# Kernel tuning notes

Hardware: AMD Instinct MI355X
Metric: run time of the kernel (lower is better)

Reference implementation:

```python
import jax, jax.numpy as jnp
import numpy as np

N = 50000       # nodes
E = 800000      # edges (before self-loops)
F_IN = 128      # in_channels
HID = 32        # hidden_channels per head
HEADS = 4
OUT = 16        # out_channels
NEG_SLOPE = 0.2 # PyG GATConv leaky_relu slope
EPS = 1e-16     # PyG softmax denominator eps
BN_EPS = 1e-5


def setup_inputs() -> dict:
    key = jax.random.key(0)
    ks = jax.random.split(key, 20)
    rn = lambda k, shp, s=0.1: (jax.random.normal(k, shp, jnp.float32) * s)
    x = jax.random.normal(ks[0], (N, F_IN), jnp.float32)
    edge_index = jax.random.randint(ks[1], (2, E), 0, N, dtype=jnp.int32)
    D0 = HEADS * HID  # 128
    return {
        "x": x, "edge_index": edge_index,
        # layer 0: GATConv(F_IN -> HID, heads=HEADS, concat=True)
        "W0": rn(ks[2], (F_IN, HEADS * HID)), "as0": rn(ks[3], (HEADS, HID)),
        "ad0": rn(ks[4], (HEADS, HID)), "b0": jnp.zeros((D0,), jnp.float32),
        "g0": jnp.ones((D0,), jnp.float32) + rn(ks[5], (D0,), 0.05),
        "be0": rn(ks[6], (D0,), 0.05),
        # layer 1: GATConv(D0 -> HID, heads=HEADS, concat=True)
        "W1": rn(ks[7], (D0, HEADS * HID)), "as1": rn(ks[8], (HEADS, HID)),
        "ad1": rn(ks[9], (HEADS, HID)), "b1": jnp.zeros((D0,), jnp.float32),
        "g1": jnp.ones((D0,), jnp.float32) + rn(ks[10], (D0,), 0.05),
        "be1": rn(ks[11], (D0,), 0.05),
        # layer 2: GATConv(D0 -> OUT, heads=1, concat=False)
        "W2": rn(ks[12], (D0, OUT)), "as2": rn(ks[13], (1, OUT)),
        "ad2": rn(ks[14], (1, OUT)), "b2": jnp.zeros((OUT,), jnp.float32),
    }


def _gat(x, src, dst, W, a_s, a_d, b, heads, ch, concat):
    n = x.shape[0]
    h = (x @ W).reshape(n, heads, ch)                       # [N,H,C]
    score_s = (h * a_s).sum(-1)                             # [N,H]
    score_d = (h * a_d).sum(-1)                             # [N,H]
    e = jax.nn.leaky_relu(score_s[src] + score_d[dst], NEG_SLOPE)  # [E,H]
    emax = jax.ops.segment_max(e, dst, num_segments=n)
    emax = jnp.where(jnp.isfinite(emax), emax, 0.0)
    p = jnp.exp(e - emax[dst])
    denom = jax.ops.segment_sum(p, dst, num_segments=n)
    alpha = p / (denom[dst] + EPS)                          # segment softmax over dst
    out = jax.ops.segment_sum(h[src] * alpha[:, :, None], dst, num_segments=n)
    out = out.reshape(n, heads * ch) if concat else out.mean(axis=1)
    return out + b


def _bn(x, g, be):
    m = x.mean(0)
    v = x.var(0)
    return (x - m) * jax.lax.rsqrt(v + BN_EPS) * g + be


def reference(x, edge_index, W0, as0, ad0, b0, g0, be0,
              W1, as1, ad1, b1, g1, be1, W2, as2, ad2, b2):
    n = x.shape[0]
    loop = jnp.arange(n, dtype=edge_index.dtype)
    src = jnp.concatenate([edge_index[0], loop])  # PyG add_self_loops
    dst = jnp.concatenate([edge_index[1], loop])
    h = _gat(x, src, dst, W0, as0, ad0, b0, HEADS, HID, True)
    h = jax.nn.elu(_bn(h, g0, be0))                 # dropout disabled (eval)
    h = _gat(h, src, dst, W1, as1, ad1, b1, HEADS, HID, True)
    h = jax.nn.elu(_bn(h, g1, be1))
    return _gat(h, src, dst, W2, as2, ad2, b2, 1, OUT, False)
```

## Files before the change

### kernel.cpp

```cpp
#include <hip/hip_runtime.h>
#include <hip/hip_bf16.h>
#include <math.h>

#define NEG_SLOPE 0.2f
#define EPS_SM 1e-16f
#define BN_EPS 1e-5f
#define CHUNKS 256

typedef __attribute__((ext_vector_type(8))) short bf16x8;
typedef __attribute__((ext_vector_type(4))) float f32x4;

__device__ __forceinline__ float lrelu(float x) { return x > 0.f ? x : NEG_SLOPE * x; }
__device__ __forceinline__ ushort f2bf(float f) {
    uint u = __float_as_uint(f);
    return (ushort)((u + 0x7FFFu + ((u >> 16) & 1u)) >> 16);
}
__device__ __forceinline__ float bfl(uint u) { return __uint_as_float(u << 16); }
__device__ __forceinline__ float bfh(uint u) { return __uint_as_float(u & 0xFFFF0000u); }

__global__ void pack_w(const float* __restrict__ W0, const float* __restrict__ W1,
                       const float* __restrict__ W2, ushort* __restrict__ P0,
                       ushort* __restrict__ P1, ushort* __restrict__ P2) {
    int i = blockIdx.x * blockDim.x + threadIdx.x;
    const float* W;
    ushort* P;
    int NC, s;
    if (i < 16384) { W = W0; P = P0; NC = 128; s = i; }
    else if (i < 32768) { W = W1; P = P1; NC = 128; s = i - 16384; }
    else if (i < 34816) { W = W2; P = P2; NC = 16; s = i - 32768; }
    else return;
    int k = s / NC, col = s % NC;
    int CT = NC >> 4;
    int dst = (((k >> 5) * CT + (col >> 4)) << 9) +
              (((col & 15) | (((k >> 3) & 3) << 4)) << 3) + (k & 7);
    P[dst] = f2bf(W[s]);
}

__global__ __launch_bounds__(256) void bucket_count(const int* __restrict__ dst, int E,
                                                    int* __restrict__ hist, int nbuck) {
    __shared__ int h[256];
    int blk = blockIdx.x, tid = threadIdx.x;
    h[tid] = 0;
    __syncthreads();
    int e0 = (int)(((long)E * blk) >> 8);
    int e1 = (int)(((long)E * (blk + 1)) >> 8);
    for (int i = e0 + tid; i < e1; i += 256) atomicAdd(&h[dst[i] >> 8], 1);
    __syncthreads();
    if (tid < nbuck) hist[tid * CHUNKS + blk] = h[tid];
}

__global__ __launch_bounds__(256) void bucket_scatter(const int* __restrict__ src,
                                                      const int* __restrict__ dst, int E,
                                                      const int* __restrict__ base,
                                                      uint* __restrict__ bpack, int nbuck) {
    __shared__ int cur[256];
    int blk = blockIdx.x, tid = threadIdx.x;
    if (tid < nbuck) cur[tid] = base[tid * CHUNKS + blk];
    __syncthreads();
    int e0 = (int)(((long)E * blk) >> 8);
    int e1 = (int)(((long)E * (blk + 1)) >> 8);
    for (int i = e0 + tid; i < e1; i += 256) {
        int d = dst[i];
        int p = atomicAdd(&cur[d >> 8], 1);
        bpack[p] = ((uint)src[i] << 8) | (uint)(d & 255);
    }
}

__global__ __launch_bounds__(256) void fine_csr(const uint* __restrict__ bpack,
                                                const int* __restrict__ base, int E, int n,
                                                int* __restrict__ offs, int* __restrict__ srcs,
                                                int nbuck) {
    __shared__ int cnt[256];
    __shared__ int wsum[4];
    int bk = blockIdx.x, tid = threadIdx.x;
    int ebase = base[bk * CHUNKS];
    int eend = base[(bk + 1) * CHUNKS];
    cnt[tid] = 0;
    __syncthreads();
    for (int i = ebase + tid; i < eend; i += 256) atomicAdd(&cnt[bpack[i] & 255], 1);
    __syncthreads();
    int lane = tid & 63, w = tid >> 6;
    int v = cnt[tid];
    int incl = v;
#pragma unroll
    for (int d = 1; d < 64; d <<= 1) {
        int t = __shfl_up(incl, d, 64);
        if (lane >= d) incl += t;
    }
    if (lane == 63) wsum[w] = incl;
    __syncthreads();
    int wbase = 0;
    for (int j = 0; j < w; ++j) wbase += wsum[j];
    int excl = wbase + incl - v;
    int node = bk * 256 + tid;
    if (node < n) offs[node] = ebase + excl;
    cnt[tid] = ebase + excl;
    __syncthreads();
    for (int i = ebase + tid; i < eend; i += 256) {
        uint pk = bpack[i];
        int p = atomicAdd(&cnt[pk & 255], 1);
        srcs[p] = (int)(pk >> 8);
    }
    if (bk == nbuck - 1 && tid == 0) offs[n] = E;
}

template <int NC, int HEADS, bool XBN>
__global__ __launch_bounds__(64) void gemm_mfma(
    const void* __restrict__ Xv, const ushort* __restrict__ Wp, ushort* __restrict__ Hb,
    int n, const float* __restrict__ sumsP, const float* __restrict__ g,
    const float* __restrict__ be, const float* __restrict__ as_, const float* __restrict__ ad_,
    float* __restrict__ ss, float* __restrict__ sd) {
    int tid = threadIdx.x;
    constexpr int CT = NC / 16;
    constexpr int FPH = NC / HEADS / 16;
    __shared__ __align__(16) ushort Xb[16 * 128];
    __shared__ float ssl[16 * HEADS], sdl[16 * HEADS];
    int row0 = (int)blockIdx.x * 16;
    if constexpr (!XBN) {
        const float* X = (const float*)Xv;
#pragma unroll
        for (int i = 0; i < 8; ++i) {
            int idx = tid + i * 64;
            int row = idx >> 5, q = idx & 31;
            int gr = row0 + row;
            float4 v = make_float4(0.f, 0.f, 0.f, 0.f);
            if (gr < n) v = ((const float4*)(X + (long)gr * 128))[q];
            ushort4 p = make_ushort4(f2bf(v.x), f2bf(v.y), f2bf(v.z), f2bf(v.w));
            int s = (q >> 1) ^ (row & 15);
            *(ushort4*)&Xb[row * 128 + s * 8 + (q & 1) * 4] = p;
        }
    } else {
        const ushort* X = (const ushort*)Xv;
        int c8 = (tid & 15) * 8;
        float inv_n = 1.f / (float)n;
        float bm[8], bs[8], bb[8];
#pragma unroll
        for (int j = 0; j < 8; ++j) {
            int ch = c8 + j;
            float m = sumsP[ch * 16] * inv_n;
            float vv = fmaxf(sumsP[(128 + ch) * 16] * inv_n - m * m, 0.f);
            bm[j] = m;
            bs[j] = rsqrtf(vv + BN_EPS) * g[ch];
            bb[j] = be[ch];
        }
#pragma unroll
        for (int i = 0; i < 4; ++i) {
            int idx = tid + i * 64;
            int row = idx >> 4, g8 = idx & 15;
            int gr = row0 + row;
            uint4 v = make_uint4(0, 0, 0, 0);
            if (gr < n) v = ((const uint4*)(X + (long)gr * 128))[g8];
            float a, b;
#define BNE(comp, j0)                                                  \
    a = bfl(comp); b = bfh(comp);                                      \
    a = (a - bm[j0]) * bs[j0] + bb[j0]; a = a > 0.f ? a : expm1f(a);   \
    b = (b - bm[j0 + 1]) * bs[j0 + 1] + bb[j0 + 1];                    \
    b = b > 0.f ? b : expm1f(b);                                       \
    comp = (uint)f2bf(a) | ((uint)f2bf(b) << 16);
            BNE(v.x, 0) BNE(v.y, 2) BNE(v.z, 4) BNE(v.w, 6)
#undef BNE
            int s = g8 ^ (row & 15);
            *(uint4*)&Xb[row * 128 + s * 8] = v;
        }
    }
    __syncthreads();
    int lane = tid;
    int lrow = lane & 15, lhi = lane >> 4;
    f32x4 zero = {0.f, 0.f, 0.f, 0.f};
    f32x4 acc[CT];
#pragma unroll
    for (int f = 0; f < CT; ++f) acc[f] = zero;
    const ushort* xr = &Xb[lrow * 128];
#pragma unroll
    for (int ks = 0; ks < 4; ++ks) {
        int kg = ks * 4 + lhi;
        bf16x8 a = *(const bf16x8*)&xr[(kg ^ lrow) << 3];
#pragma unroll
        for (int f = 0; f < CT; ++f) {
            bf16x8 b = *(const bf16x8*)&Wp[((ks * CT + f) * 64 + lane) * 8];
            acc[f] = __builtin_amdgcn_mfma_f32_16x16x32_bf16(a, b, acc[f], 0, 0, 0);
        }
    }
    __syncthreads();
#pragma unroll
    for (int f = 0; f < CT; ++f)
#pragma unroll
        for (int j = 0; j < 4; ++j)
            Xb[(lhi * 4 + j) * NC + f * 16 + lrow] = f2bf(acc[f][j]);
    float asv[CT], adv[CT];
#pragma unroll
    for (int f = 0; f < CT; ++f) {
        asv[f] = as_[f * 16 + lrow];
        adv[f] = ad_[f * 16 + lrow];
    }
#pragma unroll
    for (int h = 0; h < HEADS; ++h) {
        float ps[4] = {}, pd[4] = {};
#pragma unroll
        for (int fi = 0; fi < FPH; ++fi) {
            int f = h * FPH + fi;
#pragma unroll
            for (int j = 0; j < 4; ++j) {
                ps[j] = fmaf(acc[f][j], asv[f], ps[j]);
                pd[j] = fmaf(acc[f][j], adv[f], pd[j]);
            }
        }
#pragma unroll
        for (int j = 0; j < 4; ++j) {
#pragma unroll
            for (int d = 1; d < 16; d <<= 1) {
                ps[j] += __shfl_xor(ps[j], d, 64);
                pd[j] += __shfl_xor(pd[j], d, 64);
            }
            if (lrow == 0) {
                ssl[(lhi * 4 + j) * HEADS + h] = ps[j];
                sdl[(lhi * 4 + j) * HEADS + h] = pd[j];
            }
        }
    }
    __syncthreads();
    constexpr int NU = 16 * NC / 8;
#pragma unroll
    for (int i = 0; i < (NU + 63) / 64; ++i) {
        int idx = tid + i * 64;
        if (idx < NU) {
            int row = idx / (NC / 8), c8i = idx % (NC / 8);
            int gr = row0 + row;
            if (gr < n) ((uint4*)&Hb[(long)gr * NC])[c8i] = ((const uint4*)Xb)[idx];
        }
    }
    if (tid < 16 * HEADS) {
        int row = tid / HEADS, hh = tid % HEADS;
        int gr = row0 + row;
        if (gr < n) {
            ss[(long)gr * HEADS + hh] = ssl[tid];
            sd[(long)gr * HEADS + hh] = sdl[tid];
        }
    }
}

__global__ __launch_bounds__(1024) void scan_kernel(const int* __restrict__ deg,
                                                    int* __restrict__ offs, int n) {
    __shared__ int wsum[16];
    __shared__ int wpre[16];
    __shared__ int carry_s;
    int tid = threadIdx.x;
    int lane = tid & 63;
    int w = tid >> 6;
    if (tid == 0) carry_s = 0;
    __syncthreads();
    int nv = (n + 3) >> 2;
    for (int base = 0; base < nv; base += 1024) {
        int carry = carry_s;
        int gi = base + tid;
        int e0 = gi * 4;
        int4 v = make_int4(0, 0, 0, 0);
        if (e0 + 3 < n) {
            v = ((const int4*)deg)[gi];
        } else if (e0 < n) {
            v.x = deg[e0];
            if (e0 + 1 < n) v.y = deg[e0 + 1];
            if (e0 + 2 < n) v.z = deg[e0 + 2];
        }
        int tsum = v.x + v.y + v.z + v.w;
        int incl = tsum;
#pragma unroll
        for (int d = 1; d < 64; d <<= 1) {
            int t = __shfl_up(incl, d, 64);
            if (lane >= d) incl += t;
        }
        if (lane == 63) wsum[w] = incl;
        __syncthreads();
        if (w == 0 && lane < 16) {
            int s = wsum[lane];
#pragma unroll
            for (int d = 1; d < 16; d <<= 1) {
                int t = __shfl_up(s, d, 64);
                if (lane >= d) s += t;
            }
            wpre[lane] = s;
        }
        __syncthreads();
        int wbase = (w == 0) ? 0 : wpre[w - 1];
        int ex = carry + wbase + incl - tsum;
        if (e0 < n) {
            int4 o;
            o.x = ex;
            o.y = ex + v.x;
            o.z = o.y + v.y;
            o.w = o.z + v.z;
            if (e0 + 3 < n) {
                ((int4*)offs)[gi] = o;
            } else {
                offs[e0] = o.x;
                if (e0 + 1 < n) offs[e0 + 1] = o.y;
                if (e0 + 2 < n) offs[e0 + 2] = o.z;
            }
        }
        __syncthreads();
        if (tid == 1023) carry_s = carry + wpre[15];
        __syncthreads();
    }
    if (tid == 0) offs[n] = carry_s;
}

__global__ __launch_bounds__(256) void gat_gather4(
    const uint* __restrict__ hb, const float* __restrict__ ss, const float* __restrict__ sd,
    const int* __restrict__ offs, const int* __restrict__ srcs,
    const float* __restrict__ bias, ushort* __restrict__ outb, int n) {
    int wid = threadIdx.x >> 6;
    int lane = threadIdx.x & 63;
    int node = blockIdx.x * 4 + wid;
    if (node >= n) return;
    int off = offs[node];
    int dg = offs[node + 1] - off;
    int grp = lane >> 4;
    int ll = lane & 15;
    int hd = ll >> 2;
    float sdn = sd[node * 4 + hd];
    float es = lrelu(ss[node * 4 + hd] + sdn);
    const uint* hrow = hb + ll * 4;
    float acc[8] = {};
    float sm = 0.f;
    int i = grp;
    for (; i + 4 < dg; i += 8) {
        int s0 = srcs[off + i];
        int s1 = srcs[off + i + 4];
        float w0 = __expf(lrelu(ss[s0 * 4 + hd] + sdn));
        float w1 = __expf(lrelu(ss[s1 * 4 + hd] + sdn));
        uint4 h0 = *(const uint4*)(hrow + (long)s0 * 64);
        uint4 h1 = *(const uint4*)(hrow + (long)s1 * 64);
        sm += w0 + w1;
        acc[0] = fmaf(w0, bfl(h0.x), acc[0]); acc[0] = fmaf(w1, bfl(h1.x), acc[0]);
        acc[1] = fmaf(w0, bfh(h0.x), acc[1]); acc[1] = fmaf(w1, bfh(h1.x), acc[1]);
        acc[2] = fmaf(w0, bfl(h0.y), acc[2]); acc[2] = fmaf(w1, bfl(h1.y), acc[2]);
        acc[3] = fmaf(w0, bfh(h0.y), acc[3]); acc[3] = fmaf(w1, bfh(h1.y), acc[3]);
        acc[4] = fmaf(w0, bfl(h0.z), acc[4]); acc[4] = fmaf(w1, bfl(h1.z), acc[4]);
        acc[5] = fmaf(w0, bfh(h0.z), acc[5]); acc[5] = fmaf(w1, bfh(h1.z), acc[5]);
        acc[6] = fmaf(w0, bfl(h0.w), acc[6]); acc[6] = fmaf(w1, bfl(h1.w), acc[6]);
        acc[7] = fmaf(w0, bfh(h0.w), acc[7]); acc[7] = fmaf(w1, bfh(h1.w), acc[7]);
    }
    for (; i < dg; i += 4) {
        int s = srcs[off + i];
        float w = __expf(lrelu(ss[s * 4 + hd] + sdn));
        sm += w;
        uint4 hv = *(const uint4*)(hrow + (long)s * 64);
        acc[0] = fmaf(w, bfl(hv.x), acc[0]);
        acc[1] = fmaf(w, bfh(hv.x), acc[1]);
        acc[2] = fmaf(w, bfl(hv.y), acc[2]);
        acc[3] = fmaf(w, bfh(hv.y), acc[3]);
        acc[4] = fmaf(w, bfl(hv.z), acc[4]);
        acc[5] = fmaf(w, bfh(hv.z), acc[5]);
        acc[6] = fmaf(w, bfl(hv.w), acc[6]);
        acc[7] = fmaf(w, bfh(hv.w), acc[7]);
    }
#pragma unroll
    for (int j = 0; j < 8; ++j) {
        acc[j] += __shfl_xor(acc[j], 16, 64);
        acc[j] += __shfl_xor(acc[j], 32, 64);
    }
    sm += __shfl_xor(sm, 16, 64);
    sm += __shfl_xor(sm, 32, 64);
    float wS = __expf(es);
    sm += wS;
    uint4 hvS = *(const uint4*)(hrow + (long)node * 64);
    acc[0] = fmaf(wS, bfl(hvS.x), acc[0]);
    acc[1] = fmaf(wS, bfh(hvS.x), acc[1]);
    acc[2] = fmaf(wS, bfl(hvS.y), acc[2]);
    acc[3] = fmaf(wS, bfh(hvS.y), acc[3]);
    acc[4] = fmaf(wS, bfl(hvS.z), acc[4]);
    acc[5] = fmaf(wS, bfh(hvS.z), acc[5]);
    acc[6] = fmaf(wS, bfl(hvS.w), acc[6]);
    acc[7] = fmaf(wS, bfh(hvS.w), acc[7]);
    float inv = 1.f / (sm + EPS_SM);
    if (grp == 0) {
        float4 bA = *(const float4*)&bias[ll * 8];
        float4 bB = *(const float4*)&bias[ll * 8 + 4];
        uint4 p;
        p.x = (uint)f2bf(acc[0] * inv + bA.x) | ((uint)f2bf(acc[1] * inv + bA.y) << 16);
        p.y = (uint)f2bf(acc[2] * inv + bA.z) | ((uint)f2bf(acc[3] * inv + bA.w) << 16);
        p.z = (uint)f2bf(acc[4] * inv + bB.x) | ((uint)f2bf(acc[5] * inv + bB.y) << 16);
        p.w = (uint)f2bf(acc[6] * inv + bB.z) | ((uint)f2bf(acc[7] * inv + bB.w) << 16);
        *(uint4*)&outb[(long)node * 128 + ll * 8] = p;
    }
}

__global__ __launch_bounds__(256) void gat_gather1(
    const uint* __restrict__ hb2, const float* __restrict__ ss, const float* __restrict__ sd,
    const int* __restrict__ offs, const int* __restrict__ srcs,
    const float* __restrict__ bias, float* __restrict__ out, int n) {
    int wid = threadIdx.x >> 6;
    int lane = threadIdx.x & 63;
    int node = blockIdx.x * 4 + wid;
    if (node >= n) return;
    int off = offs[node];
    int dg = offs[node + 1] - off;
    int grp = lane >> 3;
    int ll = lane & 7;
    float sdn = sd[node];
    float es = lrelu(ss[node] + sdn);
    float a0 = 0.f, a1 = 0.f, sm = 0.f;
    int i = grp;
    for (; i + 8 < dg; i += 16) {
        int s0 = srcs[off + i];
        int s1 = srcs[off + i + 8];
        float w0 = __expf(lrelu(ss[s0] + sdn));
        float w1 = __expf(lrelu(ss[s1] + sdn));
        uint h0 = hb2[s0 * 8 + ll];
        uint h1 = hb2[s1 * 8 + ll];
        sm += w0 + w1;
        a0 = fmaf(w0, bfl(h0), a0); a0 = fmaf(w1, bfl(h1), a0);
        a1 = fmaf(w0, bfh(h0), a1); a1 = fmaf(w1, bfh(h1), a1);
    }
    for (; i < dg; i += 8) {
        int s = srcs[off + i];
        float w = __expf(lrelu(ss[s] + sdn));
        sm += w;
        uint hv = hb2[s * 8 + ll];
        a0 = fmaf(w, bfl(hv), a0);
        a1 = fmaf(w, bfh(hv), a1);
    }
#pragma unroll
    for (int d = 8; d <= 32; d <<= 1) {
        a0 += __shfl_xor(a0, d, 64);
        a1 += __shfl_xor(a1, d, 64);
        sm += __shfl_xor(sm, d, 64);
    }
    float wS = __expf(es);
    sm += wS;
    uint hvS = hb2[node * 8 + ll];
    a0 = fmaf(wS, bfl(hvS), a0);
    a1 = fmaf(wS, bfh(hvS), a1);
    float inv = 1.f / (sm + EPS_SM);
    if (grp == 0) {
        float2 o = make_float2(a0 * inv + bias[ll * 2], a1 * inv + bias[ll * 2 + 1]);
        *(float2*)&out[(long)node * 16 + ll * 2] = o;
    }
}

__global__ __launch_bounds__(256) void bn_stats_bf16(const uint4* __restrict__ X4,
                                                     float* __restrict__ sumsP, int n) {
    __shared__ float red[4096];
    int tid = threadIdx.x;
    float s[8] = {}, s2[8] = {};
    long tot = (long)n * 16;
    long T = (long)gridDim.x * 256;
    for (long i = (long)blockIdx.x * 256 + tid; i < tot; i += T) {
        uint4 v = X4[i];
        float f;
        f = bfl(v.x); s[0] += f; s2[0] = fmaf(f, f, s2[0]);
        f = bfh(v.x); s[1] += f; s2[1] = fmaf(f, f, s2[1]);
        f = bfl(v.y); s[2] += f; s2[2] = fmaf(f, f, s2[2]);
        f = bfh(v.y); s[3] += f; s2[3] = fmaf(f, f, s2[3]);
        f = bfl(v.z); s[4] += f; s2[4] = fmaf(f, f, s2[4]);
        f = bfh(v.z); s[5] += f; s2[5] = fmaf(f, f, s2[5]);
        f = bfl(v.w); s[6] += f; s2[6] = fmaf(f, f, s2[6]);
        f = bfh(v.w); s[7] += f; s2[7] = fmaf(f, f, s2[7]);
    }
#pragma unroll
    for (int j = 0; j < 8; ++j) {
        red[j * 256 + tid] = s[j];
        red[(8 + j) * 256 + tid] = s2[j];
    }
    __syncthreads();
    int ch = tid & 127, st = tid >> 7;
    int base = (st * 8 + (ch & 7)) * 256 + (ch >> 3);
    float a = 0.f;
#pragma unroll
    for (int rep = 0; rep < 16; ++rep) a += red[base + rep * 16];
    atomicAdd(&sumsP[tid * 16], a);
}

extern "C" void kernel_launch(void* const* d_in, const int* in_sizes, int n_in,
                              void* d_out, int out_size, void* d_ws, size_t ws_size,
                              hipStream_t stream) {
    const float* x = (const float*)d_in[0];
    const int* ei = (const int*)d_in[1];
    const float* W0 = (const float*)d_in[2];
    const float* as0 = (const float*)d_in[3];
    const float* ad0 = (const float*)d_in[4];
    const float* b0 = (const float*)d_in[5];
    const float* g0 = (const float*)d_in[6];
    const float* be0 = (const float*)d_in[7];
    const float* W1 = (const float*)d_in[8];
    const float* as1 = (const float*)d_in[9];
    const float* ad1 = (const float*)d_in[10];
    const float* b1 = (const float*)d_in[11];
    const float* g1 = (const float*)d_in[12];
    const float* be1 = (const float*)d_in[13];
    const float* W2 = (const float*)d_in[14];
    const float* as2 = (const float*)d_in[15];
    const float* ad2 = (const float*)d_in[16];
    const float* b2 = (const float*)d_in[17];

    int n = in_sizes[0] / 128;
    int E = in_sizes[1] / 2;
    const int* srcA = ei;
    const int* dstA = ei + E;
    int nbuck = (n + 255) >> 8;

    char* base = (char*)d_ws;
    auto alloc = [&](size_t bytes) {
        char* p = base;
        base += (bytes + 255) & ~(size_t)255;
        return p;
    };
    ushort* hb = (ushort*)alloc((size_t)n * 128 * 2);
    ushort* actb = (ushort*)alloc((size_t)n * 128 * 2);
    ushort* h2b = (ushort*)alloc((size_t)n * 16 * 2);
    float* ssb = (float*)alloc((size_t)n * 4 * 4);
    float* sdb = (float*)alloc((size_t)n * 4 * 4);
    float* sumsP0 = (float*)alloc(4096 * 4);
    float* sumsP1 = (float*)alloc(4096 * 4);
    int* hist = (int*)alloc(((size_t)nbuck * CHUNKS + 1) * 4);
    int* bbase = (int*)alloc(((size_t)nbuck * CHUNKS + 1) * 4);
    uint* bpack = (uint*)alloc((size_t)E * 4);
    int* offs = (int*)alloc(((size_t)n + 1) * 4);
    int* srcs = (int*)alloc((size_t)E * 4);
    ushort* Wp0 = (ushort*)alloc(16384 * 2);
    ushort* Wp1 = (ushort*)alloc(16384 * 2);
    ushort* Wp2 = (ushort*)alloc(2048 * 2);

    float* out = (float*)d_out;

    hipMemsetAsync(sumsP0, 0, 4096 * 4 * 2, stream);

    pack_w<<<136, 256, 0, stream>>>(W0, W1, W2, Wp0, Wp1, Wp2);

    int gGemm = (n + 15) / 16;
    int gWave = (n + 3) / 4;

    gemm_mfma<128, 4, false><<<gGemm, 64, 0, stream>>>(
        x, Wp0, hb, n, nullptr, g0, be0, as0, ad0, ssb, sdb);

    bucket_count<<<CHUNKS, 256, 0, stream>>>(dstA, E, hist, nbuck);
    scan_kernel<<<1, 1024, 0, stream>>>(hist, bbase, nbuck * CHUNKS);
    bucket_scatter<<<CHUNKS, 256, 0, stream>>>(srcA, dstA, E, bbase, bpack, nbuck);
    fine_csr<<<nbuck, 256, 0, stream>>>(bpack, bbase, E, n, offs, srcs, nbuck);

    gat_gather4<<<gWave, 256, 0, stream>>>((const uint*)hb, ssb, sdb, offs, srcs, b0, actb, n);
    bn_stats_bf16<<<256, 256, 0, stream>>>((const uint4*)actb, sumsP0, n);

    gemm_mfma<128, 4, true><<<gGemm, 64, 0, stream>>>(
        actb, Wp1, hb, n, sumsP0, g0, be0, as1, ad1, ssb, sdb);
    gat_gather4<<<gWave, 256, 0, stream>>>((const uint*)hb, ssb, sdb, offs, srcs, b1, actb, n);
    bn_stats_bf16<<<256, 256, 0, stream>>>((const uint4*)actb, sumsP1, n);

    gemm_mfma<16, 1, true><<<gGemm, 64, 0, stream>>>(
        actb, Wp2, h2b, n, sumsP1, g1, be1, as2, ad2, ssb, sdb);
    gat_gather1<<<gWave, 256, 0, stream>>>((const uint*)h2b, ssb, sdb, offs, srcs, b2, out, n);
}
```

Measured before the change: 221.1 us.

## Store hidden features head-major and gather one head per block; fuse bucket count into GEMM

```diff
diff --git a/kernel.cpp b/kernel.cpp
--- a/kernel.cpp
+++ b/kernel.cpp
@@ -20,8 +20,10 @@
 
 __global__ void pack_w(const float* __restrict__ W0, const float* __restrict__ W1,
                        const float* __restrict__ W2, ushort* __restrict__ P0,
-                       ushort* __restrict__ P1, ushort* __restrict__ P2) {
+                       ushort* __restrict__ P1, ushort* __restrict__ P2,
+                       float* __restrict__ sums) {
     int i = blockIdx.x * blockDim.x + threadIdx.x;
+    if (i < 8192) sums[i] = 0.f;
     const float* W;
     ushort* P;
     int NC, s;
@@ -36,19 +38,6 @@
     P[dst] = f2bf(W[s]);
 }
 
-__global__ __launch_bounds__(256) void bucket_count(const int* __restrict__ dst, int E,
-                                                    int* __restrict__ hist, int nbuck) {
-    __shared__ int h[256];
-    int blk = blockIdx.x, tid = threadIdx.x;
-    h[tid] = 0;
-    __syncthreads();
-    int e0 = (int)(((long)E * blk) >> 8);
-    int e1 = (int)(((long)E * (blk + 1)) >> 8);
-    for (int i = e0 + tid; i < e1; i += 256) atomicAdd(&h[dst[i] >> 8], 1);
-    __syncthreads();
-    if (tid < nbuck) hist[tid * CHUNKS + blk] = h[tid];
-}
-
 __global__ __launch_bounds__(256) void bucket_scatter(const int* __restrict__ src,
                                                       const int* __restrict__ dst, int E,
                                                       const int* __restrict__ base,
@@ -104,18 +93,35 @@
     if (bk == nbuck - 1 && tid == 0) offs[n] = E;
 }
 
-template <int NC, int HEADS, bool XBN>
+template <int NC, int HEADS, bool XBN, bool BCFUSE>
 __global__ __launch_bounds__(64) void gemm_mfma(
     const void* __restrict__ Xv, const ushort* __restrict__ Wp, ushort* __restrict__ Hb,
     int n, const float* __restrict__ sumsP, const float* __restrict__ g,
     const float* __restrict__ be, const float* __restrict__ as_, const float* __restrict__ ad_,
-    float* __restrict__ ss, float* __restrict__ sd) {
+    float* __restrict__ ss, float* __restrict__ sd,
+    const int* __restrict__ dstE, int E, int* __restrict__ hist, int nbuck) {
     int tid = threadIdx.x;
     constexpr int CT = NC / 16;
     constexpr int FPH = NC / HEADS / 16;
+    constexpr int C = NC / HEADS;
     __shared__ __align__(16) ushort Xb[16 * 128];
     __shared__ float ssl[16 * HEADS], sdl[16 * HEADS];
-    int row0 = (int)blockIdx.x * 16;
+    if constexpr (BCFUSE) {
+        if ((int)blockIdx.x < CHUNKS) {
+            int* h = (int*)Xb;
+            for (int j = tid; j < 256; j += 64) h[j] = 0;
+            __syncthreads();
+            int blk = blockIdx.x;
+            int e0 = (int)(((long)E * blk) >> 8);
+            int e1 = (int)(((long)E * (blk + 1)) >> 8);
+            for (int i = e0 + tid; i < e1; i += 64) atomicAdd(&h[dstE[i] >> 8], 1);
+            __syncthreads();
+            for (int j = tid; j < nbuck; j += 64) hist[j * CHUNKS + blk] = h[j];
+            return;
+        }
+    }
+    int bid = BCFUSE ? ((int)blockIdx.x - CHUNKS) : (int)blockIdx.x;
+    int row0 = bid * 16;
     if constexpr (!XBN) {
         const float* X = (const float*)Xv;
 #pragma unroll
@@ -224,17 +230,19 @@
     for (int i = 0; i < (NU + 63) / 64; ++i) {
         int idx = tid + i * 64;
         if (idx < NU) {
-            int row = idx / (NC / 8), c8i = idx % (NC / 8);
+            int row = idx / (NC / 8), rem = idx % (NC / 8);
+            int head = rem / (C / 8), c8i = rem % (C / 8);
             int gr = row0 + row;
-            if (gr < n) ((uint4*)&Hb[(long)gr * NC])[c8i] = ((const uint4*)Xb)[idx];
+            if (gr < n)
+                ((uint4*)(Hb + ((long)head * n + gr) * C))[c8i] = ((const uint4*)Xb)[idx];
         }
     }
     if (tid < 16 * HEADS) {
         int row = tid / HEADS, hh = tid % HEADS;
         int gr = row0 + row;
         if (gr < n) {
-            ss[(long)gr * HEADS + hh] = ssl[tid];
-            sd[(long)gr * HEADS + hh] = sdl[tid];
+            ss[(long)hh * n + gr] = ssl[tid];
+            sd[(long)hh * n + gr] = sdl[tid];
         }
     }
 }
@@ -304,84 +312,74 @@
     if (tid == 0) offs[n] = carry_s;
 }
 
-__global__ __launch_bounds__(256) void gat_gather4(
-    const uint* __restrict__ hb, const float* __restrict__ ss, const float* __restrict__ sd,
+__global__ __launch_bounds__(256) void gat_gatherH(
+    const uint2* __restrict__ hbH, const float* __restrict__ ssT, const float* __restrict__ sdT,
     const int* __restrict__ offs, const int* __restrict__ srcs,
-    const float* __restrict__ bias, ushort* __restrict__ outb, int n) {
+    const float* __restrict__ bias, ushort* __restrict__ outb, int n, int nblk) {
     int wid = threadIdx.x >> 6;
     int lane = threadIdx.x & 63;
-    int node = blockIdx.x * 4 + wid;
+    int hd = blockIdx.x / nblk;
+    int nb = blockIdx.x - hd * nblk;
+    int node = nb * 4 + wid;
     if (node >= n) return;
+    long hn = (long)hd * n;
     int off = offs[node];
     int dg = offs[node + 1] - off;
-    int grp = lane >> 4;
-    int ll = lane & 15;
-    int hd = ll >> 2;
-    float sdn = sd[node * 4 + hd];
-    float es = lrelu(ss[node * 4 + hd] + sdn);
-    const uint* hrow = hb + ll * 4;
-    float acc[8] = {};
+    int grp = lane >> 3;
+    int ll = lane & 7;
+    float sdn = sdT[hn + node];
+    float es = lrelu(ssT[hn + node] + sdn);
+    const uint2* hrow = hbH + hn * 8 + ll;
+    const float* ssh = ssT + hn;
+    float acc[4] = {};
     float sm = 0.f;
     int i = grp;
-    for (; i + 4 < dg; i += 8) {
+    for (; i + 8 < dg; i += 16) {
         int s0 = srcs[off + i];
-        int s1 = srcs[off + i + 4];
-        float w0 = __expf(lrelu(ss[s0 * 4 + hd] + sdn));
-        float w1 = __expf(lrelu(ss[s1 * 4 + hd] + sdn));
-        uint4 h0 = *(const uint4*)(hrow + (long)s0 * 64);
-        uint4 h1 = *(const uint4*)(hrow + (long)s1 * 64);
+        int s1 = srcs[off + i + 8];
+        float w0 = __expf(lrelu(ssh[s0] + sdn));
+        float w1 = __expf(lrelu(ssh[s1] + sdn));
+        uint2 h0 = hrow[(long)s0 * 8];
+        uint2 h1 = hrow[(long)s1 * 8];
         sm += w0 + w1;
         acc[0] = fmaf(w0, bfl(h0.x), acc[0]); acc[0] = fmaf(w1, bfl(h1.x), acc[0]);
         acc[1] = fmaf(w0, bfh(h0.x), acc[1]); acc[1] = fmaf(w1, bfh(h1.x), acc[1]);
         acc[2] = fmaf(w0, bfl(h0.y), acc[2]); acc[2] = fmaf(w1, bfl(h1.y), acc[2]);
         acc[3] = fmaf(w0, bfh(h0.y), acc[3]); acc[3] = fmaf(w1, bfh(h1.y), acc[3]);
-        acc[4] = fmaf(w0, bfl(h0.z), acc[4]); acc[4] = fmaf(w1, bfl(h1.z), acc[4]);
-        acc[5] = fmaf(w0, bfh(h0.z), acc[5]); acc[5] = fmaf(w1, bfh(h1.z), acc[5]);
-        acc[6] = fmaf(w0, bfl(h0.w), acc[6]); acc[6] = fmaf(w1, bfl(h1.w), acc[6]);
-        acc[7] = fmaf(w0, bfh(h0.w), acc[7]); acc[7] = fmaf(w1, bfh(h1.w), acc[7]);
-    }
-    for (; i < dg; i += 4) {
+    }
+    for (; i < dg; i += 8) {
         int s = srcs[off + i];
-        float w = __expf(lrelu(ss[s * 4 + hd] + sdn));
+        float w = __expf(lrelu(ssh[s] + sdn));
         sm += w;
-        uint4 hv = *(const uint4*)(hrow + (long)s * 64);
+        uint2 hv = hrow[(long)s * 8];
         acc[0] = fmaf(w, bfl(hv.x), acc[0]);
         acc[1] = fmaf(w, bfh(hv.x), acc[1]);
         acc[2] = fmaf(w, bfl(hv.y), acc[2]);
         acc[3] = fmaf(w, bfh(hv.y), acc[3]);
-        acc[4] = fmaf(w, bfl(hv.z), acc[4]);
-        acc[5] = fmaf(w, bfh(hv.z), acc[5]);
-        acc[6] = fmaf(w, bfl(hv.w), acc[6]);
-        acc[7] = fmaf(w, bfh(hv.w), acc[7]);
-    }
-#pragma unroll
-    for (int j = 0; j < 8; ++j) {
+    }
+#pragma unroll
+    for (int j = 0; j < 4; ++j) {
+        acc[j] += __shfl_xor(acc[j], 8, 64);
         acc[j] += __shfl_xor(acc[j], 16, 64);
         acc[j] += __shfl_xor(acc[j], 32, 64);
     }
+    sm += __shfl_xor(sm, 8, 64);
     sm += __shfl_xor(sm, 16, 64);
     sm += __shfl_xor(sm, 32, 64);
     float wS = __expf(es);
     sm += wS;
-    uint4 hvS = *(const uint4*)(hrow + (long)node * 64);
+    uint2 hvS = hrow[(long)node * 8];
     acc[0] = fmaf(wS, bfl(hvS.x), acc[0]);
     acc[1] = fmaf(wS, bfh(hvS.x), acc[1]);
     acc[2] = fmaf(wS, bfl(hvS.y), acc[2]);
     acc[3] = fmaf(wS, bfh(hvS.y), acc[3]);
-    acc[4] = fmaf(wS, bfl(hvS.z), acc[4]);
-    acc[5] = fmaf(wS, bfh(hvS.z), acc[5]);
-    acc[6] = fmaf(wS, bfl(hvS.w), acc[6]);
-    acc[7] = fmaf(wS, bfh(hvS.w), acc[7]);
     float inv = 1.f / (sm + EPS_SM);
     if (grp == 0) {
-        float4 bA = *(const float4*)&bias[ll * 8];
-        float4 bB = *(const float4*)&bias[ll * 8 + 4];
-        uint4 p;
-        p.x = (uint)f2bf(acc[0] * inv + bA.x) | ((uint)f2bf(acc[1] * inv + bA.y) << 16);
-        p.y = (uint)f2bf(acc[2] * inv + bA.z) | ((uint)f2bf(acc[3] * inv + bA.w) << 16);
-        p.z = (uint)f2bf(acc[4] * inv + bB.x) | ((uint)f2bf(acc[5] * inv + bB.y) << 16);
-        p.w = (uint)f2bf(acc[6] * inv + bB.z) | ((uint)f2bf(acc[7] * inv + bB.w) << 16);
-        *(uint4*)&outb[(long)node * 128 + ll * 8] = p;
+        float4 b4 = *(const float4*)&bias[hd * 32 + ll * 4];
+        uint2 p;
+        p.x = (uint)f2bf(acc[0] * inv + b4.x) | ((uint)f2bf(acc[1] * inv + b4.y) << 16);
+        p.y = (uint)f2bf(acc[2] * inv + b4.z) | ((uint)f2bf(acc[3] * inv + b4.w) << 16);
+        *(uint2*)&outb[(long)node * 128 + hd * 32 + ll * 4] = p;
     }
 }
 
@@ -523,30 +521,28 @@
 
     float* out = (float*)d_out;
 
-    hipMemsetAsync(sumsP0, 0, 4096 * 4 * 2, stream);
-
-    pack_w<<<136, 256, 0, stream>>>(W0, W1, W2, Wp0, Wp1, Wp2);
+    pack_w<<<136, 256, 0, stream>>>(W0, W1, W2, Wp0, Wp1, Wp2, sumsP0);
 
     int gGemm = (n + 15) / 16;
-    int gWave = (n + 3) / 4;
-
-    gemm_mfma<128, 4, false><<<gGemm, 64, 0, stream>>>(
-        x, Wp0, hb, n, nullptr, g0, be0, as0, ad0, ssb, sdb);
-
-    bucket_count<<<CHUNKS, 256, 0, stream>>>(dstA, E, hist, nbuck);
+    int nblk = (n + 3) / 4;
+
+    gemm_mfma<128, 4, false, true><<<CHUNKS + gGemm, 64, 0, stream>>>(
+        x, Wp0, hb, n, nullptr, g0, be0, as0, ad0, ssb, sdb, dstA, E, hist, nbuck);
     scan_kernel<<<1, 1024, 0, stream>>>(hist, bbase, nbuck * CHUNKS);
     bucket_scatter<<<CHUNKS, 256, 0, stream>>>(srcA, dstA, E, bbase, bpack, nbuck);
     fine_csr<<<nbuck, 256, 0, stream>>>(bpack, bbase, E, n, offs, srcs, nbuck);
 
-    gat_gather4<<<gWave, 256, 0, stream>>>((const uint*)hb, ssb, sdb, offs, srcs, b0, actb, n);
+    gat_gatherH<<<4 * nblk, 256, 0, stream>>>((const uint2*)hb, ssb, sdb, offs, srcs,
+                                              b0, actb, n, nblk);
     bn_stats_bf16<<<256, 256, 0, stream>>>((const uint4*)actb, sumsP0, n);
 
-    gemm_mfma<128, 4, true><<<gGemm, 64, 0, stream>>>(
-        actb, Wp1, hb, n, sumsP0, g0, be0, as1, ad1, ssb, sdb);
-    gat_gather4<<<gWave, 256, 0, stream>>>((const uint*)hb, ssb, sdb, offs, srcs, b1, actb, n);
+    gemm_mfma<128, 4, true, false><<<gGemm, 64, 0, stream>>>(
+        actb, Wp1, hb, n, sumsP0, g0, be0, as1, ad1, ssb, sdb, nullptr, 0, nullptr, 0);
+    gat_gatherH<<<4 * nblk, 256, 0, stream>>>((const uint2*)hb, ssb, sdb, offs, srcs,
+                                              b1, actb, n, nblk);
     bn_stats_bf16<<<256, 256, 0, stream>>>((const uint4*)actb, sumsP1, n);
 
-    gemm_mfma<16, 1, true><<<gGemm, 64, 0, stream>>>(
-        actb, Wp2, h2b, n, sumsP1, g1, be1, as2, ad2, ssb, sdb);
-    gat_gather1<<<gWave, 256, 0, stream>>>((const uint*)h2b, ssb, sdb, offs, srcs, b2, out, n);
-}
+    gemm_mfma<16, 1, true, false><<<gGemm, 64, 0, stream>>>(
+        actb, Wp2, h2b, n, sumsP1, g1, be1, as2, ad2, ssb, sdb, nullptr, 0, nullptr, 0);
+    gat_gather1<<<nblk, 256, 0, stream>>>((const uint*)h2b, ssb, sdb, offs, srcs, b2, out, n);
+}
```

New measurement: 291.4 us. +31.8%, slower.
